# Kernel tuning notes

Measured on AMD Instinct MI355X. Metric: run time of the kernel, lower is better.

## Reference

```python
import jax, jax.numpy as jnp
import numpy as np

LATENT_DIM = 256
BOOK_SIZE = 8192


def setup_inputs() -> dict:
    key = jax.random.key(0)
    k1, k2 = jax.random.split(key)
    z_e = jax.random.normal(k1, (16, LATENT_DIM, 32, 32), dtype=jnp.float32)
    codebook = jax.random.normal(k2, (BOOK_SIZE, LATENT_DIM), dtype=jnp.float32)
    return {"z_e": z_e, "codebook": codebook}


def reference(z_e, codebook):
    # NCHW -> NHWC -> (B*H*W, D)
    flat_z = jnp.transpose(z_e, (0, 2, 3, 1)).reshape(-1, LATENT_DIM)
    # squared euclidean distance via matmul: ||z||^2 + ||e||^2 - 2 z.e
    dist = (
        jnp.sum(flat_z ** 2, axis=1, keepdims=True)
        + jnp.sum(codebook ** 2, axis=1)
        - 2.0 * flat_z @ codebook.T
    )  # (N, book_size)
    indices = jnp.argmin(dist, axis=1)          # (N,)
    z_q = codebook[indices]                      # (N, D) gather
    return z_q, indices
```

## Files before the change

kernel.cpp:

```cpp
#include <hip/hip_runtime.h>
#include <stdint.h>

#define NROWS 16384
#define NCODES 8192
#define DIM 256
#define EPS_S 0.4f
#define SM 0.8f

typedef __attribute__((ext_vector_type(8))) short bf16x8;
typedef __attribute__((ext_vector_type(16))) float f32x16;
typedef unsigned int uint32;

__device__ __forceinline__ unsigned short f2bf(float f) {
  union { float f; unsigned int u; } v; v.f = f;
  unsigned int u = v.u;
  return (unsigned short)((u + 0x7FFFu + ((u >> 16) & 1u)) >> 16);
}

__device__ __forceinline__ unsigned long long packdi(float d, int idx) {
  unsigned int u = __float_as_uint(d);
  u = (u & 0x80000000u) ? ~u : (u | 0x80000000u);
  return ((unsigned long long)u << 32) | (unsigned int)idx;
}
__device__ __forceinline__ unsigned long long u64min(unsigned long long a,
                                                     unsigned long long b) {
  return a < b ? a : b;
}
__device__ __forceinline__ unsigned long long shflx64(unsigned long long v, int m) {
  int lo = __shfl_xor((int)(unsigned int)v, m);
  int hi = __shfl_xor((int)(v >> 32), m);
  return ((unsigned long long)(unsigned int)hi << 32) | (unsigned int)lo;
}
__device__ __forceinline__ uint32 umax(uint32 a, uint32 b) { return a > b ? a : b; }
__device__ __forceinline__ uint32 umin(uint32 a, uint32 b) { return a < b ? a : b; }

__global__ __launch_bounds__(256) void prep(const float* __restrict__ z,
                                            const float* __restrict__ cb,
                                            float* __restrict__ flatz,
                                            ushort* __restrict__ zb,
                                            ushort* __restrict__ eb,
                                            float* __restrict__ enorm) {
  __shared__ float t[32][33];
  const int blk = blockIdx.x;
  if (blk < 4096) {
    const int tx = threadIdx.x & 31, ty = threadIdx.x >> 5;
    const int ht = blk & 31, ct = (blk >> 5) & 7, b = blk >> 8;
    const float* src = z + (size_t)b * 262144 + (size_t)(ct * 32) * 1024 + ht * 32;
#pragma unroll
    for (int i = 0; i < 4; ++i) {
      int c = ty + i * 8;
      t[c][tx] = src[c * 1024 + tx];
    }
    __syncthreads();
#pragma unroll
    for (int i = 0; i < 4; ++i) {
      int hw = ty + i * 8;
      int row = b * 1024 + ht * 32 + hw;
      float v = t[tx][hw];
      flatz[(size_t)row * 256 + ct * 32 + tx] = v;
      zb[(size_t)row * 256 + ct * 32 + tx] = f2bf(v);
    }
  } else {
    const int lane = threadIdx.x & 63, wave = threadIdx.x >> 6;
    const int code = (blk - 4096) * 4 + wave;
    float4 v = *(const float4*)(cb + (size_t)code * 256 + lane * 4);
    ushort4 o;
    o.x = f2bf(v.x); o.y = f2bf(v.y); o.z = f2bf(v.z); o.w = f2bf(v.w);
    *(ushort4*)(eb + (size_t)code * 256 + lane * 4) = o;
    float ss = v.x * v.x + v.y * v.y + v.z * v.z + v.w * v.w;
#pragma unroll
    for (int s = 1; s < 64; s <<= 1) ss += __shfl_xor(ss, s);
    if (lane == 0) enorm[code] = ss;
  }
}

__global__ __launch_bounds__(256) void vq_gemm(const ushort* __restrict__ eb,
                                               const ushort* __restrict__ zb,
                                               const float* __restrict__ enorm,
                                               uint32* __restrict__ bm) {
  __shared__ __align__(16) ushort As[2][4096];
  __shared__ __align__(16) ushort Bs[2][4096];
  const int tid = threadIdx.x;
  const int wave = tid >> 6, lane = tid & 63;
  const int wr = wave >> 1, wc = wave & 1;
  const int code0 = blockIdx.x * 128;
  const int zrow0 = blockIdx.y * 128;
  const int l31 = lane & 31, lg = lane >> 5;

  f32x16 acc[2][2];
#pragma unroll
  for (int i = 0; i < 2; ++i) {
    const float* ep = enorm + code0 + wr * 64 + i * 32 + 4 * lg;
    float4 e0 = *(const float4*)(ep);
    float4 e1 = *(const float4*)(ep + 8);
    float4 e2 = *(const float4*)(ep + 16);
    float4 e3 = *(const float4*)(ep + 24);
    f32x16 c0;
    c0[0]  = 1024.f - 0.5f * e0.x; c0[1]  = 1024.f - 0.5f * e0.y;
    c0[2]  = 1024.f - 0.5f * e0.z; c0[3]  = 1024.f - 0.5f * e0.w;
    c0[4]  = 1024.f - 0.5f * e1.x; c0[5]  = 1024.f - 0.5f * e1.y;
    c0[6]  = 1024.f - 0.5f * e1.z; c0[7]  = 1024.f - 0.5f * e1.w;
    c0[8]  = 1024.f - 0.5f * e2.x; c0[9]  = 1024.f - 0.5f * e2.y;
    c0[10] = 1024.f - 0.5f * e2.z; c0[11] = 1024.f - 0.5f * e2.w;
    c0[12] = 1024.f - 0.5f * e3.x; c0[13] = 1024.f - 0.5f * e3.y;
    c0[14] = 1024.f - 0.5f * e3.z; c0[15] = 1024.f - 0.5f * e3.w;
    acc[i][0] = c0; acc[i][1] = c0;
  }

  const int r_in = lane >> 2;
  const int kc = (lane & 3) ^ ((lane >> 3) & 3);
  const ushort* aG0 = eb + (size_t)(code0 + wave * 16 + r_in) * 256 + kc * 8;
  const ushort* aG1 = eb + (size_t)(code0 + 64 + wave * 16 + r_in) * 256 + kc * 8;
  const ushort* bG0 = zb + (size_t)(zrow0 + wave * 16 + r_in) * 256 + kc * 8;
  const ushort* bG1 = zb + (size_t)(zrow0 + 64 + wave * 16 + r_in) * 256 + kc * 8;
  const int wo0 = wave * 512 + lane * 8;
  const int wo1 = (wave + 4) * 512 + lane * 8;

  bf16x8 pa[2], pb[2], na[2], nb[2];
  pa[0] = *(const bf16x8*)(aG0);        pa[1] = *(const bf16x8*)(aG1);
  pb[0] = *(const bf16x8*)(bG0);        pb[1] = *(const bf16x8*)(bG1);
  na[0] = *(const bf16x8*)(aG0 + 32);   na[1] = *(const bf16x8*)(aG1 + 32);
  nb[0] = *(const bf16x8*)(bG0 + 32);   nb[1] = *(const bf16x8*)(bG1 + 32);
  *(bf16x8*)(&As[0][wo0]) = pa[0];
  *(bf16x8*)(&As[0][wo1]) = pa[1];
  *(bf16x8*)(&Bs[0][wo0]) = pb[0];
  *(bf16x8*)(&Bs[0][wo1]) = pb[1];
  __syncthreads();

  const int ra = wr * 64 + l31;
  const int rb = wc * 64 + l31;
  const int hash = (l31 >> 1) & 3;

#pragma unroll
  for (int k0 = 0; k0 < 8; ++k0) {
    const int cur = k0 & 1;
    const int kn = (k0 + 2 <= 7) ? (k0 + 2) : 7;
    bf16x8 qa0 = *(const bf16x8*)(aG0 + kn * 32);
    bf16x8 qa1 = *(const bf16x8*)(aG1 + kn * 32);
    bf16x8 qb0 = *(const bf16x8*)(bG0 + kn * 32);
    bf16x8 qb1 = *(const bf16x8*)(bG1 + kn * 32);
    if (k0 < 7) {
      *(bf16x8*)(&As[cur ^ 1][wo0]) = na[0];
      *(bf16x8*)(&As[cur ^ 1][wo1]) = na[1];
      *(bf16x8*)(&Bs[cur ^ 1][wo0]) = nb[0];
      *(bf16x8*)(&Bs[cur ^ 1][wo1]) = nb[1];
    }
    bf16x8 af[2][2], bf[2][2];
#pragma unroll
    for (int i = 0; i < 2; ++i)
#pragma unroll
      for (int h = 0; h < 2; ++h) {
        int slot = (h * 2 + lg) ^ hash;
        af[i][h] = *(const bf16x8*)(&As[cur][(ra + i * 32) * 32 + slot * 8]);
        bf[i][h] = *(const bf16x8*)(&Bs[cur][(rb + i * 32) * 32 + slot * 8]);
      }
#pragma unroll
    for (int h = 0; h < 2; ++h)
#pragma unroll
      for (int i = 0; i < 2; ++i)
#pragma unroll
        for (int j = 0; j < 2; ++j)
          acc[i][j] = __builtin_amdgcn_mfma_f32_32x32x16_bf16(
              af[i][h], bf[j][h], acc[i][j], 0, 0, 0);
    na[0] = qa0; na[1] = qa1; nb[0] = qb0; nb[1] = qb1;
    __syncthreads();
  }

  const int cid0 = blockIdx.x * 8 + wr * 4;
#pragma unroll
  for (int j = 0; j < 2; ++j) {
    uint32 res[4];
#pragma unroll
    for (int i = 0; i < 2; ++i)
#pragma unroll
      for (int hc = 0; hc < 2; ++hc) {
        uint32 m1 = 0, m2 = 0;
#pragma unroll
        for (int p = 0; p < 8; ++p) {
          uint32 id = (uint32)((p & 3) | (lg << 2) | ((p >> 2) << 3));
          uint32 pv = (__float_as_uint(acc[i][j][hc * 8 + p]) & ~31u) | id;
          m2 = umax(m2, umin(m1, pv));
          m1 = umax(m1, pv);
        }
        uint32 o1 = (uint32)__shfl_xor((int)m1, 32);
        uint32 o2 = (uint32)__shfl_xor((int)m2, 32);
        m2 = umax(umax(m2, o2), umin(m1, o1));
        m1 = umax(m1, o1);
        float s1 = __uint_as_float(m1 & ~31u);
        float s2 = __uint_as_float(m2 & ~31u);
        res[i * 2 + hc] = (s1 - s2 > SM) ? (m1 | 16u) : m1;
      }
    if (lane < 32) {
      int zr = zrow0 + wc * 64 + j * 32 + l31;
      uint4 o; o.x = res[0]; o.y = res[1]; o.z = res[2]; o.w = res[3];
      *(uint4*)(bm + (size_t)zr * 512 + cid0) = o;
    }
  }
}

__device__ __forceinline__ unsigned long long chunk_exact(
    int chunk, const float* __restrict__ zrow, const float* __restrict__ cb,
    const float* __restrict__ enorm, int lane) {
  const int code = chunk * 16 + (lane >> 2);
  const float* zp = zrow + (lane & 3) * 64;
  const float* cp = cb + (size_t)code * 256 + (lane & 3) * 64;
  float s = 0.f;
#pragma unroll
  for (int d = 0; d < 64; d += 4) {
    float4 zv = *(const float4*)(zp + d);
    float4 cv = *(const float4*)(cp + d);
    s = fmaf(zv.x, cv.x, s); s = fmaf(zv.y, cv.y, s);
    s = fmaf(zv.z, cv.z, s); s = fmaf(zv.w, cv.w, s);
  }
  s += __shfl_xor(s, 1);
  s += __shfl_xor(s, 2);
  float dist = fmaf(-2.f, s, enorm[code]);
  unsigned long long key = ((lane & 3) == 0) ? packdi(dist, code) : ~0ull;
#pragma unroll
  for (int m = 1; m < 64; m <<= 1) key = u64min(key, shflx64(key, m));
  return key;
}

__global__ __launch_bounds__(256) void vq_sel(const uint32* __restrict__ bm,
                                              const float* __restrict__ flatz,
                                              const float* __restrict__ cb,
                                              const float* __restrict__ enorm,
                                              float* __restrict__ zq,
                                              float* __restrict__ oidx) {
  const int lane = threadIdx.x & 63;
  const int row = blockIdx.x * 4 + (threadIdx.x >> 6);
  uint4 va = *(const uint4*)(bm + (size_t)row * 512 + lane * 8);
  uint4 vb = *(const uint4*)(bm + (size_t)row * 512 + lane * 8 + 4);
  uint32 v[8] = {va.x, va.y, va.z, va.w, vb.x, vb.y, vb.z, vb.w};
  uint32 m1 = 0, m2 = 0; int ch = 0;
#pragma unroll
  for (int s = 0; s < 8; ++s) {
    uint32 pv = v[s];
    m2 = umax(m2, umin(m1, pv));
    ch = (pv > m1) ? (lane * 8 + s) : ch;
    m1 = umax(m1, pv);
  }
#pragma unroll
  for (int m = 1; m < 64; m <<= 1) {
    uint32 o1 = (uint32)__shfl_xor((int)m1, m);
    uint32 o2 = (uint32)__shfl_xor((int)m2, m);
    int oc = __shfl_xor(ch, m);
    m2 = umax(umax(m2, o2), umin(m1, o1));
    ch = (o1 > m1) ? oc : ch;
    m1 = umax(m1, o1);
  }
  float s1 = __uint_as_float(m1 & ~31u);
  float s2 = __uint_as_float(m2 & ~31u);
  int idx;
  if ((m1 & 16u) && (s1 - s2 > SM)) {
    idx = ch * 16 + (int)(m1 & 15u);
  } else {
    const float* zrow = flatz + (size_t)row * 256;
    unsigned long long key = chunk_exact(ch, zrow, cb, enorm, lane);
    float dbest;
    { unsigned int u = (unsigned int)(key >> 32);
      u = (u & 0x80000000u) ? (u & 0x7FFFFFFFu) : ~u;
      dbest = __uint_as_float(u); }
    float thr = (1024.f - 0.5f * dbest) - EPS_S;
#pragma unroll
    for (int s = 0; s < 8; ++s) {
      bool cand = __uint_as_float(v[s] & ~31u) >= thr;
      unsigned long long mk = __ballot(cand);
      while (mk) {
        int L = __ffsll(mk) - 1;
        mk &= mk - 1;
        int c2 = L * 8 + s;
        if (c2 == ch) continue;
        key = u64min(key, chunk_exact(c2, zrow, cb, enorm, lane));
      }
    }
    idx = (int)(key & 0xFFFFFFFFull);
  }
  if (lane == 0) oidx[row] = (float)idx;
  float4 val = *(const float4*)(cb + (size_t)idx * 256 + lane * 4);
  *(float4*)(zq + (size_t)row * 256 + lane * 4) = val;
}

extern "C" void kernel_launch(void* const* d_in, const int* in_sizes, int n_in,
                              void* d_out, int out_size, void* d_ws, size_t ws_size,
                              hipStream_t stream) {
  const float* z = (const float*)d_in[0];
  const float* cb = (const float*)d_in[1];
  char* ws = (char*)d_ws;
  ushort* zb = (ushort*)(ws);
  ushort* eb = (ushort*)(ws + (8u << 20));
  float* enorm = (float*)(ws + (12u << 20));
  uint32* bm = (uint32*)(ws + (13u << 20));
  float* zq = (float*)d_out;
  float* oidx = zq + (size_t)NROWS * DIM;
  float* flatz = zq;

  prep<<<4096 + NCODES / 4, 256, 0, stream>>>(z, cb, flatz, zb, eb, enorm);
  vq_gemm<<<dim3(NCODES / 128, NROWS / 128), 256, 0, stream>>>(eb, zb, enorm, bm);
  vq_sel<<<NROWS / 4, 256, 0, stream>>>(bm, flatz, cb, enorm, zq, oidx);
}
```

Baseline: 194.2 us.

## Enlarge GEMM tile to 256x256 with direct global-to-LDS loads and phased MFMA

Rewrites the bf16 distance GEMM to use 256x256 output tiles per 512-thread block, with K steps of 64 double-buffered in LDS. Tiles are filled with global_load_lds (direct to shared memory) instead of going through registers, and the MFMA work is split into four sub-phases with barriers and setprio so loads interleave with compute. The aim is more operand reuse per byte loaded and fewer register staging copies. The cost is 128KB of LDS per block, which limits occupancy, plus extra barrier overhead.

```diff
diff --git a/kernel.cpp b/kernel.cpp
--- a/kernel.cpp
+++ b/kernel.cpp
@@ -33,6 +33,12 @@
 }
 __device__ __forceinline__ uint32 umax(uint32 a, uint32 b) { return a > b ? a : b; }
 __device__ __forceinline__ uint32 umin(uint32 a, uint32 b) { return a < b ? a : b; }
+
+__device__ __forceinline__ void glds16(const ushort* g, ushort* l) {
+  __builtin_amdgcn_global_load_lds(
+      (const __attribute__((address_space(1))) unsigned int*)g,
+      (__attribute__((address_space(3))) unsigned int*)l, 16, 0, 0);
+}
 
 __global__ __launch_bounds__(256) void prep(const float* __restrict__ z,
                                             const float* __restrict__ cb,
@@ -74,23 +80,34 @@
   }
 }
 
-__global__ __launch_bounds__(256) void vq_gemm(const ushort* __restrict__ eb,
-                                               const ushort* __restrict__ zb,
-                                               const float* __restrict__ enorm,
-                                               uint32* __restrict__ bm) {
-  __shared__ __align__(16) ushort As[2][4096];
-  __shared__ __align__(16) ushort Bs[2][4096];
-  const int tid = threadIdx.x;
-  const int wave = tid >> 6, lane = tid & 63;
-  const int wr = wave >> 1, wc = wave & 1;
-  const int code0 = blockIdx.x * 128;
-  const int zrow0 = blockIdx.y * 128;
+__global__ __launch_bounds__(512, 2) void vq_gemm(const ushort* __restrict__ eb,
+                                                  const ushort* __restrict__ zb,
+                                                  const float* __restrict__ enorm,
+                                                  uint32* __restrict__ bm) {
+  __shared__ __align__(16) ushort As[2][16384];
+  __shared__ __align__(16) ushort Bs[2][16384];
+  const int wave = threadIdx.x >> 6, lane = threadIdx.x & 63;
+  const int wm = wave >> 2, wn = wave & 3;
   const int l31 = lane & 31, lg = lane >> 5;
-
-  f32x16 acc[2][2];
-#pragma unroll
-  for (int i = 0; i < 2; ++i) {
-    const float* ep = enorm + code0 + wr * 64 + i * 32 + 4 * lg;
+  const int code0 = blockIdx.x * 256;
+  const int zrow0 = blockIdx.y * 256;
+
+  const int srow = wave * 8 + (lane >> 3);
+  const int sslot = (lane & 7) ^ ((lane >> 3) & 7);
+  const ushort* aSrc = eb + (size_t)(code0 + srow) * 256 + sslot * 8;
+  const ushort* bSrc = zb + (size_t)(zrow0 + srow) * 256 + sslot * 8;
+  const int ldst = wave * 512;
+
+#pragma unroll
+  for (int r = 0; r < 4; ++r) {
+    glds16(aSrc + r * 16384, &As[0][r * 4096 + ldst]);
+    glds16(bSrc + r * 16384, &Bs[0][r * 4096 + ldst]);
+  }
+
+  f32x16 acc[4][2];
+#pragma unroll
+  for (int m = 0; m < 4; ++m) {
+    const float* ep = enorm + code0 + wm * 128 + m * 32 + 4 * lg;
     float4 e0 = *(const float4*)(ep);
     float4 e1 = *(const float4*)(ep + 8);
     float4 e2 = *(const float4*)(ep + 16);
@@ -104,81 +121,119 @@
     c0[10] = 1024.f - 0.5f * e2.z; c0[11] = 1024.f - 0.5f * e2.w;
     c0[12] = 1024.f - 0.5f * e3.x; c0[13] = 1024.f - 0.5f * e3.y;
     c0[14] = 1024.f - 0.5f * e3.z; c0[15] = 1024.f - 0.5f * e3.w;
-    acc[i][0] = c0; acc[i][1] = c0;
-  }
-
-  const int r_in = lane >> 2;
-  const int kc = (lane & 3) ^ ((lane >> 3) & 3);
-  const ushort* aG0 = eb + (size_t)(code0 + wave * 16 + r_in) * 256 + kc * 8;
-  const ushort* aG1 = eb + (size_t)(code0 + 64 + wave * 16 + r_in) * 256 + kc * 8;
-  const ushort* bG0 = zb + (size_t)(zrow0 + wave * 16 + r_in) * 256 + kc * 8;
-  const ushort* bG1 = zb + (size_t)(zrow0 + 64 + wave * 16 + r_in) * 256 + kc * 8;
-  const int wo0 = wave * 512 + lane * 8;
-  const int wo1 = (wave + 4) * 512 + lane * 8;
-
-  bf16x8 pa[2], pb[2], na[2], nb[2];
-  pa[0] = *(const bf16x8*)(aG0);        pa[1] = *(const bf16x8*)(aG1);
-  pb[0] = *(const bf16x8*)(bG0);        pb[1] = *(const bf16x8*)(bG1);
-  na[0] = *(const bf16x8*)(aG0 + 32);   na[1] = *(const bf16x8*)(aG1 + 32);
-  nb[0] = *(const bf16x8*)(bG0 + 32);   nb[1] = *(const bf16x8*)(bG1 + 32);
-  *(bf16x8*)(&As[0][wo0]) = pa[0];
-  *(bf16x8*)(&As[0][wo1]) = pa[1];
-  *(bf16x8*)(&Bs[0][wo0]) = pb[0];
-  *(bf16x8*)(&Bs[0][wo1]) = pb[1];
+    acc[m][0] = c0; acc[m][1] = c0;
+  }
+
   __syncthreads();
 
-  const int ra = wr * 64 + l31;
-  const int rb = wc * 64 + l31;
-  const int hash = (l31 >> 1) & 3;
-
-#pragma unroll
-  for (int k0 = 0; k0 < 8; ++k0) {
-    const int cur = k0 & 1;
-    const int kn = (k0 + 2 <= 7) ? (k0 + 2) : 7;
-    bf16x8 qa0 = *(const bf16x8*)(aG0 + kn * 32);
-    bf16x8 qa1 = *(const bf16x8*)(aG1 + kn * 32);
-    bf16x8 qb0 = *(const bf16x8*)(bG0 + kn * 32);
-    bf16x8 qb1 = *(const bf16x8*)(bG1 + kn * 32);
-    if (k0 < 7) {
-      *(bf16x8*)(&As[cur ^ 1][wo0]) = na[0];
-      *(bf16x8*)(&As[cur ^ 1][wo1]) = na[1];
-      *(bf16x8*)(&Bs[cur ^ 1][wo0]) = nb[0];
-      *(bf16x8*)(&Bs[cur ^ 1][wo1]) = nb[1];
-    }
-    bf16x8 af[2][2], bf[2][2];
-#pragma unroll
-    for (int i = 0; i < 2; ++i)
-#pragma unroll
-      for (int h = 0; h < 2; ++h) {
-        int slot = (h * 2 + lg) ^ hash;
-        af[i][h] = *(const bf16x8*)(&As[cur][(ra + i * 32) * 32 + slot * 8]);
-        bf[i][h] = *(const bf16x8*)(&Bs[cur][(rb + i * 32) * 32 + slot * 8]);
-      }
-#pragma unroll
-    for (int h = 0; h < 2; ++h)
-#pragma unroll
-      for (int i = 0; i < 2; ++i)
-#pragma unroll
-        for (int j = 0; j < 2; ++j)
-          acc[i][j] = __builtin_amdgcn_mfma_f32_32x32x16_bf16(
-              af[i][h], bf[j][h], acc[i][j], 0, 0, 0);
-    na[0] = qa0; na[1] = qa1; nb[0] = qb0; nb[1] = qb1;
-    __syncthreads();
-  }
-
-  const int cid0 = blockIdx.x * 8 + wr * 4;
-#pragma unroll
-  for (int j = 0; j < 2; ++j) {
-    uint32 res[4];
-#pragma unroll
-    for (int i = 0; i < 2; ++i)
+  int col[4];
+#pragma unroll
+  for (int ks = 0; ks < 4; ++ks)
+    col[ks] = ((((ks << 1) | lg) ^ (lane & 7)) << 3);
+  const int arow = (wm * 128 + l31) * 64;
+  const int brow = (wn * 64 + l31) * 64;
+
+  bf16x8 ab[2][4];
+  bf16x8 bb0[4], bb1[4];
+
+#pragma unroll
+  for (int t = 0; t < 4; ++t) {
+    const int cur = t & 1;
+    const ushort* A = As[cur];
+    const ushort* B = Bs[cur];
+    ushort* An = As[cur ^ 1];
+    ushort* Bn = Bs[cur ^ 1];
+    const int ko = (t + 1) * 64;
+
+#pragma unroll
+    for (int mi = 0; mi < 2; ++mi)
+#pragma unroll
+      for (int ks = 0; ks < 4; ++ks)
+        ab[mi][ks] = *(const bf16x8*)(A + arow + mi * 2048 + col[ks]);
+#pragma unroll
+    for (int ks = 0; ks < 4; ++ks)
+      bb0[ks] = *(const bf16x8*)(B + brow + col[ks]);
+    if (t < 3) {
+      glds16(aSrc + 0 * 16384 + ko, An + 0 * 4096 + ldst);
+      glds16(aSrc + 1 * 16384 + ko, An + 1 * 4096 + ldst);
+      glds16(bSrc + 0 * 16384 + ko, Bn + 0 * 4096 + ldst);
+      glds16(bSrc + 1 * 16384 + ko, Bn + 1 * 4096 + ldst);
+    }
+    __builtin_amdgcn_s_barrier();
+    __builtin_amdgcn_s_setprio(1);
+#pragma unroll
+    for (int ks = 0; ks < 4; ++ks) {
+      acc[0][0] = __builtin_amdgcn_mfma_f32_32x32x16_bf16(ab[0][ks], bb0[ks],
+                                                          acc[0][0], 0, 0, 0);
+      acc[1][0] = __builtin_amdgcn_mfma_f32_32x32x16_bf16(ab[1][ks], bb0[ks],
+                                                          acc[1][0], 0, 0, 0);
+    }
+    __builtin_amdgcn_s_setprio(0);
+    __builtin_amdgcn_s_barrier();
+
+#pragma unroll
+    for (int ks = 0; ks < 4; ++ks)
+      bb1[ks] = *(const bf16x8*)(B + brow + 2048 + col[ks]);
+    if (t < 3) {
+      glds16(aSrc + 2 * 16384 + ko, An + 2 * 4096 + ldst);
+      glds16(aSrc + 3 * 16384 + ko, An + 3 * 4096 + ldst);
+      glds16(bSrc + 2 * 16384 + ko, Bn + 2 * 4096 + ldst);
+      glds16(bSrc + 3 * 16384 + ko, Bn + 3 * 4096 + ldst);
+    }
+    __builtin_amdgcn_s_barrier();
+    __builtin_amdgcn_s_setprio(1);
+#pragma unroll
+    for (int ks = 0; ks < 4; ++ks) {
+      acc[0][1] = __builtin_amdgcn_mfma_f32_32x32x16_bf16(ab[0][ks], bb1[ks],
+                                                          acc[0][1], 0, 0, 0);
+      acc[1][1] = __builtin_amdgcn_mfma_f32_32x32x16_bf16(ab[1][ks], bb1[ks],
+                                                          acc[1][1], 0, 0, 0);
+    }
+    __builtin_amdgcn_s_setprio(0);
+    __builtin_amdgcn_s_barrier();
+
+#pragma unroll
+    for (int mi = 0; mi < 2; ++mi)
+#pragma unroll
+      for (int ks = 0; ks < 4; ++ks)
+        ab[mi][ks] = *(const bf16x8*)(A + arow + (2 + mi) * 2048 + col[ks]);
+    __builtin_amdgcn_s_barrier();
+    __builtin_amdgcn_s_setprio(1);
+#pragma unroll
+    for (int ks = 0; ks < 4; ++ks) {
+      acc[2][1] = __builtin_amdgcn_mfma_f32_32x32x16_bf16(ab[0][ks], bb1[ks],
+                                                          acc[2][1], 0, 0, 0);
+      acc[3][1] = __builtin_amdgcn_mfma_f32_32x32x16_bf16(ab[1][ks], bb1[ks],
+                                                          acc[3][1], 0, 0, 0);
+    }
+    __builtin_amdgcn_s_setprio(0);
+    __builtin_amdgcn_s_barrier();
+
+    __builtin_amdgcn_s_setprio(1);
+#pragma unroll
+    for (int ks = 0; ks < 4; ++ks) {
+      acc[2][0] = __builtin_amdgcn_mfma_f32_32x32x16_bf16(ab[0][ks], bb0[ks],
+                                                          acc[2][0], 0, 0, 0);
+      acc[3][0] = __builtin_amdgcn_mfma_f32_32x32x16_bf16(ab[1][ks], bb0[ks],
+                                                          acc[3][0], 0, 0, 0);
+    }
+    __builtin_amdgcn_s_setprio(0);
+    if (t < 3) __syncthreads();
+  }
+
+  const int cid0 = blockIdx.x * 16 + wm * 8;
+#pragma unroll
+  for (int n = 0; n < 2; ++n) {
+    uint32 res[8];
+#pragma unroll
+    for (int m = 0; m < 4; ++m)
 #pragma unroll
       for (int hc = 0; hc < 2; ++hc) {
         uint32 m1 = 0, m2 = 0;
 #pragma unroll
         for (int p = 0; p < 8; ++p) {
           uint32 id = (uint32)((p & 3) | (lg << 2) | ((p >> 2) << 3));
-          uint32 pv = (__float_as_uint(acc[i][j][hc * 8 + p]) & ~31u) | id;
+          uint32 pv = (__float_as_uint(acc[m][n][hc * 8 + p]) & ~31u) | id;
           m2 = umax(m2, umin(m1, pv));
           m1 = umax(m1, pv);
         }
@@ -188,13 +243,15 @@
         m1 = umax(m1, o1);
         float s1 = __uint_as_float(m1 & ~31u);
         float s2 = __uint_as_float(m2 & ~31u);
-        res[i * 2 + hc] = (s1 - s2 > SM) ? (m1 | 16u) : m1;
+        res[m * 2 + hc] = (s1 - s2 > SM) ? (m1 | 16u) : m1;
       }
-    if (lane < 32) {
-      int zr = zrow0 + wc * 64 + j * 32 + l31;
-      uint4 o; o.x = res[0]; o.y = res[1]; o.z = res[2]; o.w = res[3];
-      *(uint4*)(bm + (size_t)zr * 512 + cid0) = o;
-    }
+    const int zr = zrow0 + wn * 64 + n * 32 + l31;
+    uint4 o;
+    o.x = lg ? res[4] : res[0];
+    o.y = lg ? res[5] : res[1];
+    o.z = lg ? res[6] : res[2];
+    o.w = lg ? res[7] : res[3];
+    *(uint4*)(bm + (size_t)zr * 512 + cid0 + lg * 4) = o;
   }
 }
 
@@ -296,6 +353,6 @@
   float* flatz = zq;
 
   prep<<<4096 + NCODES / 4, 256, 0, stream>>>(z, cb, flatz, zb, eb, enorm);
-  vq_gemm<<<dim3(NCODES / 128, NROWS / 128), 256, 0, stream>>>(eb, zb, enorm, bm);
+  vq_gemm<<<dim3(NCODES / 256, NROWS / 256), 512, 0, stream>>>(eb, zb, enorm, bm);
   vq_sel<<<NROWS / 4, 256, 0, stream>>>(bm, flatz, cb, enorm, zq, oidx);
 }
```

Result: slower. 199.7 us (+2.8%).
